# Performance work log

Measured on AMD Instinct MI355X. Metric: run time of the kernel, lower is better.

## Reference

```python
import jax, jax.numpy as jnp
import numpy as np
import math

B, T = 8, 16
CODE_NUM = 1024
CODE_SIZE = 48
GRAPH_SIZE = 32
HIDDEN = 150      # hidden_size == t_output_size
T_ATTN = 32       # t_attention_size
DP_ATTN = 32      # DotProductAttention size
OUT = 1024


def _lin(k, fan_in, fan_out):
    s = 1.0 / math.sqrt(fan_in)
    kw, kb = jax.random.split(k)
    W = jax.random.uniform(kw, (fan_in, fan_out), minval=-s, maxval=s, dtype=jnp.float32)
    b = jax.random.uniform(kb, (fan_out,), minval=-s, maxval=s, dtype=jnp.float32)
    return W, b


def setup_inputs():
    key = jax.random.key(0)
    ks = jax.random.split(key, 16)
    u = jax.random.uniform(ks[0], (B, T, CODE_NUM))
    m1 = (u < 0.03).astype(jnp.float32)                   # persistent codes
    m2 = ((u >= 0.03) & (u < 0.05)).astype(jnp.float32)   # emerging neighbor codes
    m3 = ((u >= 0.05) & (u < 0.06)).astype(jnp.float32)   # emerging unrelated codes
    divided = jnp.stack([m1, m2, m3], axis=-1)            # [B,T,N,3], disjoint
    code_x = jnp.clip(m1 + m2 + m3, 0.0, 1.0)             # current-visit codes
    neighbors = ((u >= 0.06) & (u < 0.12)).astype(jnp.float32)
    lens = jax.random.randint(ks[1], (B,), T // 2, T + 1)
    a = (jax.random.uniform(ks[2], (CODE_NUM, CODE_NUM)) < 0.01).astype(jnp.float32)
    adj = a / (a.sum(axis=1, keepdims=True) + 1e-6)
    c_emb = jax.random.normal(ks[3], (CODE_NUM, CODE_SIZE)) * 0.05
    n_emb = jax.random.normal(ks[4], (CODE_NUM, CODE_SIZE)) * 0.05
    u_emb = jax.random.normal(ks[5], (CODE_NUM, GRAPH_SIZE)) * 0.05
    Wg, bg = _lin(ks[6], CODE_SIZE, GRAPH_SIZE)           # GraphLayer dense
    Wi, bi = _lin(ks[7], GRAPH_SIZE, 3 * HIDDEN)          # GRUCell input (r|z|n)
    Wh, bh = _lin(ks[8], HIDDEN, 3 * HIDDEN)              # GRUCell hidden (r|z|n)
    Wq, bq = _lin(ks[9], GRAPH_SIZE, T_ATTN)
    Wk, bk = _lin(ks[10], GRAPH_SIZE, T_ATTN)
    Wv, bv = _lin(ks[11], GRAPH_SIZE, HIDDEN)
    Wd, bd = _lin(ks[12], HIDDEN, DP_ATTN)                # DotProductAttention dense
    context = jax.random.normal(ks[13], (DP_ATTN,)) * 0.1
    Wc, bc = _lin(ks[14], HIDDEN, OUT)                    # Classifier
    return dict(code_x=code_x, divided=divided, neighbors=neighbors, lens=lens,
                adj=adj, c_emb=c_emb, n_emb=n_emb, u_emb=u_emb, Wg=Wg, bg=bg,
                Wi=Wi, bi=bi, Wh=Wh, bh=bh, Wq=Wq, bq=bq, Wk=Wk, bk=bk,
                Wv=Wv, bv=bv, Wd=Wd, bd=bd, context=context, Wc=Wc, bc=bc)


def _forward(code_x, divided, neighbors, lens, adj, c_emb, n_emb, u_emb,
             Wg, bg, Wi, bi, Wh, bh, Wq, bq, Wk, bk, Wv, bv, Wd, bd, context, Wc, bc):
    Bb, Tt, N = code_x.shape
    H = Wh.shape[0]
    NEG = -1e30
    scale = 1.0 / math.sqrt(Wq.shape[1])

    def step(carry, xs):
        h_prev, no_prev = carry                 # [B,N,H], [B,N,G]
        c_t, d_t, n_t, t_idx = xs               # [B,N], [B,N,3], [B,N], scalar
        c = c_t[..., None]
        nb = n_t[..., None]
        # GraphLayer: masked embeddings + one-hop adjacency aggregation
        ce = c * c_emb                           # [B,N,C]
        ne = nb * n_emb
        adj_ce = jnp.einsum('mn,bnc->bmc', adj, ce)
        adj_ne = jnp.einsum('mn,bnc->bmc', adj, ne)
        co = jax.nn.leaky_relu((ce + c * adj_ce + c * adj_ne) @ Wg + bg)      # [B,N,G]
        no = jax.nn.leaky_relu((ne + nb * adj_ne + nb * adj_ce) @ Wg + bg)

        m1 = d_t[..., 0]; m2 = d_t[..., 1]; m3 = d_t[..., 2]
        # TransitionLayer part 1: GRUCell on persistent (m1) codes; h_new starts at 0
        gi = co @ Wi + bi
        gh = h_prev @ Wh + bh
        i_r, i_z, i_n = jnp.split(gi, 3, axis=-1)
        h_r, h_z, h_n = jnp.split(gh, 3, axis=-1)
        r = jax.nn.sigmoid(i_r + h_r)
        z = jax.nn.sigmoid(i_z + h_z)
        n_g = jnp.tanh(i_n + r * h_n)
        h_m1 = (1.0 - z) * n_g + z * h_prev
        h_new = jnp.where(m1[..., None] > 0, h_m1, 0.0)

        # TransitionLayer part 2: single-head attention over emerging (m2|m3) codes, t>0
        m23 = (m2 + m3) > 0
        qrows = jnp.where(m2[..., None] > 0, no_prev,
                          jnp.where(m3[..., None] > 0, u_emb, 0.0))           # [B,N,G]
        q = qrows @ Wq + bq
        k = co @ Wk + bk
        v = qrows @ Wv + bv
        s = jnp.einsum('bia,bja->bij', q, k) * scale
        s = jnp.where(m23[:, None, :], s, NEG)   # keys restricted to m2|m3 set
        h_m23 = jnp.tanh(jnp.einsum('bij,bjh->bih', jax.nn.softmax(s, axis=-1), v))
        use23 = t_idx > 0
        h_new = jnp.where(jnp.logical_and(use23, m23)[..., None], h_m23, h_new)

        # per-step output: max-pool over each active subset (0 if subset empty)
        om1 = jnp.max(jnp.where(m1[..., None] > 0, h_m1, NEG), axis=1)
        om1 = jnp.where(jnp.any(m1 > 0, axis=1)[:, None], om1, 0.0)
        om23 = jnp.max(jnp.where(m23[..., None], h_m23, NEG), axis=1)
        om23 = jnp.where(jnp.logical_and(use23, jnp.any(m23, axis=1))[:, None], om23, 0.0)
        return (h_new, no), om1 + om23

    h0 = jnp.zeros((Bb, N, H), code_x.dtype)
    no0 = jnp.zeros((Bb, N, Wg.shape[1]), code_x.dtype)
    xs = (jnp.moveaxis(code_x, 1, 0), jnp.moveaxis(divided, 1, 0),
          jnp.moveaxis(neighbors, 1, 0), jnp.arange(Tt))
    _, outs = jax.lax.scan(step, (h0, no0), xs)
    outs = jnp.moveaxis(outs, 0, 1)              # [B,T,H]

    # DotProductAttention over (ragged) visit axis
    vu = (outs @ Wd + bd) @ context              # [B,T]
    tmask = jnp.arange(Tt)[None, :] < lens[:, None]
    score = jax.nn.softmax(jnp.where(tmask, vu, NEG), axis=-1)
    pooled = jnp.einsum('bth,bt->bh', outs, score)
    # Classifier (dropout_rate=0 -> identity) with sigmoid activation
    return jax.nn.sigmoid(pooled @ Wc + bc)


def reference(code_x, divided, neighbors, lens, adj, c_emb, n_emb, u_emb,
              Wg, bg, Wi, bi, Wh, bh, Wq, bq, Wk, bk, Wv, bv, Wd, bd, context, Wc, bc):
    return _forward(code_x, divided, neighbors, lens, adj, c_emb, n_emb, u_emb,
                    Wg, bg, Wi, bi, Wh, bh, Wq, bq, Wk, bk, Wv, bv, Wd, bd,
                    context, Wc, bc)
```

## Files before the change

kernel.cpp:

```cpp
#include <hip/hip_runtime.h>
#include <hip/hip_bf16.h>

#define Bq   8
#define Tq   16
#define Nq   1024
#define Cq   48
#define Gq   32
#define Hq   150
#define H3q  450
#define TAq  32
#define OUTq 1024
#define BTq  128

#define NC_CAP 128
#define NM_CAP 64
#define NACT   (2 * NC_CAP)
#define MTILE  16
#define NMH    (NM_CAP / 2)

__device__ __forceinline__ float lrelu(float x){ return x > 0.f ? x : 0.01f * x; }
__device__ __forceinline__ float sigm(float x){ return 1.f / (1.f + expf(-x)); }

__device__ int   g_n1[BTq], g_n23[BTq], g_nchain[BTq], g_nchain2[BTq];
__device__ short g_list1[BTq][NM_CAP];
__device__ short g_list23[BTq][NM_CAP];
__device__ short g_mapc[BTq][Nq];
__device__ short g_mapn[BTq][Nq];
__device__ int   g_chain[BTq][NM_CAP];
__device__ int   g_chain2[BTq][NM_CAP];
__device__ unsigned char g_cls[BTq][NM_CAP];
__device__ float g_Pc[Nq][Gq];
__device__ float g_Pn[Nq][Gq];
__device__ float g_co[BTq][NC_CAP][Gq];
__device__ float g_no[BTq][NC_CAP][Gq];
__device__ float g_hm23[BTq][NM_CAP][Hq];
__device__ float g_om23p2[2][BTq][Hq];
__device__ float g_hm1[BTq][NM_CAP][Hq];
__device__ float g_om1p2[2][BTq][Hq];
__device__ float g_om1c[BTq][Hq];

__device__ __forceinline__ void gi3(const float* co_row, const float* Wi, const float* bi, int h,
                                    float& gr, float& gz, float& gn){
    gr = bi[h]; gz = bi[Hq + h]; gn = bi[2 * Hq + h];
    #pragma unroll
    for (int g = 0; g < Gq; ++g){
        float c = co_row[g];
        const float* w = Wi + g * H3q + h;
        gr += c * w[0];
        gz += c * w[Hq];
        gn += c * w[2 * Hq];
    }
}

__global__ __launch_bounds__(256) void k_pre(const float* c_emb, const float* n_emb, const float* Wg){
    int idx   = blockIdx.x * 256 + threadIdx.x;
    int which = idx >> 15;
    int r     = (idx >> 5) & 1023;
    int g     = idx & 31;
    const float* emb = which ? n_emb : c_emb;
    float acc = 0.f;
    for (int c = 0; c < Cq; ++c)
        acc += emb[r * Cq + c] * Wg[c * Gq + g];
    if (which) g_Pn[r][g] = acc; else g_Pc[r][g] = acc;
}

__global__ __launch_bounds__(512) void k_co(const float* code_x, const float* neighbors,
                                            const float* adj, const float* bg){
    int bt = blockIdx.x >> 1, half = blockIdx.x & 1, tid = threadIdx.x;
    __shared__ unsigned char cf_s[Nq], nf_s[Nq];
    __shared__ short lc_s[NC_CAP], ln_s[NC_CAP];
    __shared__ short act_s[NACT];
    __shared__ int nc_s, nn_s;
    __shared__ float Pact_s[NACT][Gq];
    __shared__ float A_s[MTILE][NACT];
    __shared__ short mrow_s[MTILE];
    int wave = tid >> 6, lane = tid & 63;

    for (int n = tid; n < Nq; n += 512){
        cf_s[n] = (code_x[bt * Nq + n]    > 0.f) ? 1 : 0;
        nf_s[n] = (neighbors[bt * Nq + n] > 0.f) ? 1 : 0;
    }
    __syncthreads();
    if (wave == 0){
        int base = 0;
        for (int start = 0; start < Nq; start += 64){
            int n = start + lane;
            int pred = cf_s[n];
            unsigned long long mm = __ballot(pred != 0);
            int pos = base + (int)__popcll(mm & ((1ull << lane) - 1ull));
            if (pred && pos < NC_CAP) lc_s[pos] = (short)n;
            base += (int)__popcll(mm);
        }
        if (lane == 0) nc_s = min(base, NC_CAP);
    } else if (wave == 1){
        int base = 0;
        for (int start = 0; start < Nq; start += 64){
            int n = start + lane;
            int pred = nf_s[n];
            unsigned long long mm = __ballot(pred != 0);
            int pos = base + (int)__popcll(mm & ((1ull << lane) - 1ull));
            if (pred && pos < NC_CAP) ln_s[pos] = (short)n;
            base += (int)__popcll(mm);
        }
        if (lane == 0) nn_s = min(base, NC_CAP);
    } else {
        if (half == 0) for (int n = tid - 128; n < Nq; n += 384) g_mapc[bt][n] = -1;
        else           for (int n = tid - 128; n < Nq; n += 384) g_mapn[bt][n] = -1;
    }
    __syncthreads();
    int nc = nc_s, nn = nn_s, total = nc + nn;

    for (int i = tid; i < total; i += 512) act_s[i] = (i < nc) ? lc_s[i] : ln_s[i - nc];
    if (half == 0) for (int i = tid; i < nc; i += 512) g_mapc[bt][lc_s[i]] = (short)i;
    else           for (int i = tid; i < nn; i += 512) g_mapn[bt][ln_s[i]] = (short)i;
    __syncthreads();

    for (int idx = tid; idx < total * Gq; idx += 512){
        int i = idx >> 5, g = idx & 31;
        Pact_s[i][g] = (i < nc) ? g_Pc[act_s[i]][g] : g_Pn[act_s[i]][g];
    }
    __syncthreads();

    int g = tid & 31, grp = tid >> 5;
    float bgv = bg[g];
    for (int rbase = half; rbase < total; rbase += 2 * MTILE){
        if (tid < MTILE){
            int r = rbase + 2 * tid;
            mrow_s[tid] = (r < total) ? act_s[r] : 0;
        }
        __syncthreads();
        int ntile = min(MTILE, (total - rbase + 1) / 2);
        for (int idx = tid; idx < ntile * total; idx += 512){
            int ti = idx / total, j = idx % total;
            A_s[ti][j] = adj[(size_t)mrow_s[ti] * Nq + act_s[j]];
        }
        __syncthreads();
        if (grp < ntile){
            int r = rbase + 2 * grp;
            float agg = 0.f;
            #pragma unroll 4
            for (int j = 0; j < total; ++j) agg += A_s[grp][j] * Pact_s[j][g];
            float v = lrelu(Pact_s[r][g] + agg + bgv);
            if (r < nc) g_co[bt][r][g]      = v;
            else        g_no[bt][r - nc][g] = v;
        }
        __syncthreads();
    }
}

__global__ __launch_bounds__(512) void k_mid(const float* divided, const float* u_emb,
                                             const float* Wk, const float* bk,
                                             const float* Wq_, const float* bq_,
                                             const float* Wv_, const float* bv_,
                                             const float* bg){
    int bt = blockIdx.x >> 1, half = blockIdx.x & 1, tid = threadIdx.x;
    int t = bt % Tq, btp = bt - 1;
    __shared__ unsigned char f1_s[Nq], f2_s[Nq], f3_s[Nq];
    __shared__ short l1_s[NM_CAP], l23_s[NM_CAP];
    __shared__ unsigned char wm_s[NMH];
    __shared__ int n1_s, n23_s;
    __shared__ float co23_s[NM_CAP][Gq];
    __shared__ float qr_s[NM_CAP][Gq];
    __shared__ float q_s[NMH][TAq + 1];
    __shared__ float k_s[NM_CAP][TAq + 1];
    __shared__ float s_s[NMH][NM_CAP + 1];
    __shared__ float vv_s[NM_CAP][Hq];
    __shared__ float hm_s[NMH][Hq];
    int wave = tid >> 6, lane = tid & 63;

    for (int idx = tid; idx < Nq * 3; idx += 512){
        float v = divided[(size_t)bt * Nq * 3 + idx];
        int n = idx / 3, c = idx - n * 3;
        unsigned char f = (v > 0.f) ? 1 : 0;
        if (c == 0) f1_s[n] = f;
        else if (c == 1) f2_s[n] = f;
        else f3_s[n] = f;
    }
    __syncthreads();
    if (wave == 0){
        int base = 0;
        for (int start = 0; start < Nq; start += 64){
            int n = start + lane;
            int pred = f1_s[n];
            unsigned long long mm = __ballot(pred != 0);
            int pos = base + (int)__popcll(mm & ((1ull << lane) - 1ull));
            if (pred && pos < NM_CAP) l1_s[pos] = (short)n;
            base += (int)__popcll(mm);
        }
        if (lane == 0) n1_s = min(base, NM_CAP);
    } else if (wave == 1){
        int base = 0;
        for (int start = 0; start < Nq; start += 64){
            int n = start + lane;
            int m2 = f2_s[n], m3 = f3_s[n];
            int pred = m2 | m3;
            unsigned long long mm = __ballot(pred != 0);
            int pos = base + (int)__popcll(mm & ((1ull << lane) - 1ull));
            if (pred && pos < NM_CAP) l23_s[pos] = (short)(n | (m2 ? 0x400 : 0));
            base += (int)__popcll(mm);
        }
        if (lane == 0) n23_s = min(base, NM_CAP);
    }
    __syncthreads();
    int n1 = n1_s, n23 = n23_s;
    if (half == 0){
        for (int i = tid; i < n1;  i += 512) g_list1[bt][i]  = l1_s[i];
        for (int i = tid; i < n23; i += 512) g_list23[bt][i] = l23_s[i];
        if (tid == 0){ g_n1[bt] = n1; g_n23[bt] = n23; }
    }
    if (t == 0 || n23 == 0) return;
    int nMy = (n23 > half) ? ((n23 - half + 1) >> 1) : 0;

    for (int il = tid; il < nMy; il += 512){
        int row = l23_s[2 * il + half] & 1023;
        unsigned char wm = 0;
        if (t < Tq - 1) wm = (divided[((size_t)(bt + 1) * Nq + row) * 3] > 0.f) ? 1 : 0;
        wm_s[il] = wm;
    }
    for (int idx = tid; idx < n23 * Gq; idx += 512){
        int i = idx >> 5, g = idx & 31;
        co23_s[i][g] = g_co[bt][g_mapc[bt][l23_s[i] & 1023]][g];
    }
    for (int idx = tid; idx < n23 * Gq; idx += 512){
        int i = idx >> 5, g = idx & 31;
        int e = l23_s[i], row = e & 1023;
        float qv;
        if (e & 0x400){
            int slot = g_mapn[btp][row];
            qv = (slot >= 0) ? g_no[btp][slot][g] : lrelu(bg[g]);
        } else {
            qv = u_emb[row * Gq + g];
        }
        qr_s[i][g] = qv;
    }
    __syncthreads();
    for (int idx = tid; idx < n23 * TAq; idx += 512){
        int i = idx >> 5, a = idx & 31;
        float acck = bk[a];
        #pragma unroll
        for (int g = 0; g < Gq; ++g) acck += co23_s[i][g] * Wk[g * TAq + a];
        k_s[i][a] = acck;
    }
    for (int idx = tid; idx < nMy * TAq; idx += 512){
        int il = idx >> 5, a = idx & 31;
        int i = 2 * il + half;
        float accq = bq_[a];
        #pragma unroll
        for (int g = 0; g < Gq; ++g) accq += qr_s[i][g] * Wq_[g * TAq + a];
        q_s[il][a] = accq;
    }
    for (int idx = tid; idx < n23 * Hq; idx += 512){
        int i = idx / Hq, h = idx % Hq;
        float acc = bv_[h];
        #pragma unroll
        for (int g = 0; g < Gq; ++g) acc += qr_s[i][g] * Wv_[g * Hq + h];
        vv_s[i][h] = acc;
    }
    __syncthreads();

    const float scale = 0.17677669529663687f;
    for (int idx = tid; idx < nMy * n23; idx += 512){
        int il = idx / n23, j = idx % n23;
        float acc = 0.f;
        #pragma unroll
        for (int a = 0; a < TAq; ++a) acc += q_s[il][a] * k_s[j][a];
        s_s[il][j] = acc * scale;
    }
    __syncthreads();
    for (int il = tid; il < nMy; il += 512){
        float mx = -1e30f;
        for (int j = 0; j < n23; ++j) mx = fmaxf(mx, s_s[il][j]);
        float sum = 0.f;
        for (int j = 0; j < n23; ++j){ float e = expf(s_s[il][j] - mx); s_s[il][j] = e; sum += e; }
        float inv = 1.f / sum;
        for (int j = 0; j < n23; ++j) s_s[il][j] *= inv;
    }
    __syncthreads();
    for (int idx = tid; idx < nMy * Hq; idx += 512){
        int il = idx / Hq, h = idx % Hq;
        float acc = 0.f;
        for (int j = 0; j < n23; ++j) acc += s_s[il][j] * vv_s[j][h];
        hm_s[il][h] = tanhf(acc);
    }
    __syncthreads();
    for (int idx = tid; idx < nMy * Hq; idx += 512){
        int il = idx / Hq, h = idx % Hq;
        if (wm_s[il]) g_hm23[bt][2 * il + half][h] = hm_s[il][h];
    }
    for (int h = tid; h < Hq; h += 512){
        float mx = -1e30f;
        for (int il = 0; il < nMy; ++il) mx = fmaxf(mx, hm_s[il][h]);
        g_om23p2[half][bt][h] = mx;
    }
}

__global__ __launch_bounds__(512) void k_gru1(const float* Wi, const float* bi,
                                              const float* Wh, const float* bh){
    int bt = blockIdx.x >> 1, half = blockIdx.x & 1, tid = threadIdx.x;
    int t = bt % Tq, btp = bt - 1;
    __shared__ short map1p[Nq], map23p[Nq];
    __shared__ short l1_s[NM_CAP];
    __shared__ unsigned char cls_s[NM_CAP];
    __shared__ int m23l_s[NM_CAP];
    __shared__ int nf23_s;
    __shared__ float co1_s[NMH][Gq];
    __shared__ float hb_s[Hq];
    __shared__ float ghf_s[H3q];
    __shared__ float gi_s[NMH][H3q];
    int n1 = g_n1[bt];
    int nMy = (n1 > half) ? ((n1 - half + 1) >> 1) : 0;
    for (int n = tid; n < Nq; n += 512){ map1p[n] = -1; map23p[n] = -1; }
    for (int i = tid; i < n1; i += 512) l1_s[i] = g_list1[bt][i];
    __syncthreads();
    if (t >= 1){
        int n1p = g_n1[btp];
        for (int i = tid; i < n1p; i += 512) map1p[g_list1[btp][i]] = (short)i;
        if (t >= 2){
            int n23p = g_n23[btp];
            for (int i = tid; i < n23p; i += 512) map23p[g_list23[btp][i] & 1023] = (short)i;
        }
    }
    __syncthreads();
    if (tid < 64){
        int i = tid;
        int cls = 0, sp = -1;
        if (i < n1 && t >= 1){
            int row = l1_s[i];
            if (map1p[row] >= 0){ cls = 1; sp = map1p[row]; }
            else if (t >= 2 && map23p[row] >= 0){ cls = 2; sp = map23p[row]; }
        }
        if (i < n1) cls_s[i] = (unsigned char)cls;
        if (half == 0 && i < n1) g_cls[bt][i] = (unsigned char)cls;
        unsigned long long mch = __ballot(cls == 1);
        unsigned long long m23 = __ballot(cls == 2 && (i & 1) == half);
        int pch = (int)__popcll(mch & ((1ull << i) - 1ull));
        int p23 = (int)__popcll(m23 & ((1ull << i) - 1ull));
        if (half == 0 && cls == 1) g_chain[bt][pch] = (i << 16) | sp;
        if (cls == 2 && (i & 1) == half) m23l_s[p23] = (i << 16) | sp;
        if (i == 0){
            nf23_s = (int)__popcll(m23);
            if (half == 0) g_nchain[bt] = (int)__popcll(mch);
        }
    }
    for (int idx = tid; idx < nMy * Gq; idx += 512){
        int il = idx >> 5, g = idx & 31;
        co1_s[il][g] = g_co[bt][g_mapc[bt][l1_s[2 * il + half]]][g];
    }
    __syncthreads();

    if (tid < H3q){
        float wcol[Gq];
        #pragma unroll
        for (int g = 0; g < Gq; ++g) wcol[g] = Wi[g * H3q + tid];
        float bij = bi[tid];
        for (int il = 0; il < nMy; ++il){
            float acc = bij;
            #pragma unroll
            for (int g = 0; g < Gq; ++g) acc += co1_s[il][g] * wcol[g];
            gi_s[il][tid] = acc;
        }
    }
    __syncthreads();

    for (int idx = tid; idx < nMy * Hq; idx += 512){
        int il = idx / Hq, h = idx % Hq;
        int i = 2 * il + half;
        if (cls_s[i] != 0) continue;
        float gr = gi_s[il][h], gz = gi_s[il][Hq + h], gn = gi_s[il][2 * Hq + h];
        float r  = sigm(gr + bh[h]);
        float z  = sigm(gz + bh[Hq + h]);
        float ng = tanhf(gn + r * bh[2 * Hq + h]);
        gi_s[il][h] = (1.f - z) * ng;
    }
    __syncthreads();

    int nf23 = nf23_s;
    for (int f = 0; f < nf23; ++f){
        int pk = m23l_s[f]; int i = pk >> 16, sp = pk & 0xffff;
        int il = i >> 1;
        for (int h = tid; h < Hq; h += 512) hb_s[h] = g_hm23[btp][sp][h];
        __syncthreads();
        for (int j = tid; j < H3q; j += 512){
            float acc = bh[j];
            for (int k2 = 0; k2 < Hq; ++k2) acc += hb_s[k2] * Wh[k2 * H3q + j];
            ghf_s[j] = acc;
        }
        __syncthreads();
        for (int h = tid; h < Hq; h += 512){
            float gr = gi_s[il][h], gz = gi_s[il][Hq + h], gn = gi_s[il][2 * Hq + h];
            float r  = sigm(gr + ghf_s[h]);
            float z  = sigm(gz + ghf_s[Hq + h]);
            float ng = tanhf(gn + r * ghf_s[2 * Hq + h]);
            gi_s[il][h] = (1.f - z) * ng + z * hb_s[h];
        }
        __syncthreads();
    }

    for (int idx = tid; idx < nMy * Hq; idx += 512){
        int il = idx / Hq, h = idx % Hq;
        int i = 2 * il + half;
        if (cls_s[i] != 1) g_hm1[bt][i][h] = gi_s[il][h];
    }
    for (int h = tid; h < Hq; h += 512){
        float mx = -1e30f;
        for (int il = 0; il < nMy; ++il)
            if (cls_s[2 * il + half] != 1) mx = fmaxf(mx, gi_s[il][h]);
        g_om1p2[half][bt][h] = mx;
    }
}

__global__ __launch_bounds__(512) void k_gru1b(const float* Wi, const float* bi,
                                               const float* Wh, const float* bh){
    int bt = blockIdx.x, tid = threadIdx.x;
    int t = bt % Tq, btp = bt - 1;
    __shared__ unsigned char defer_s[NM_CAP];
    __shared__ float co_s[Gq];
    __shared__ float hb_s[Hq];
    __shared__ float ghf_s[H3q];
    __shared__ float cmax_s[Hq];
    int nch = (t > 0) ? g_nchain[bt] : 0;
    for (int h = tid; h < Hq; h += 512) cmax_s[h] = -1e30f;
    if (tid < 64){
        int c = tid;
        int defer = 0;
        if (c < nch){
            int sp = g_chain[bt][c] & 0xffff;
            defer = (g_cls[btp][sp] == 1) ? 1 : 0;
            defer_s[c] = (unsigned char)defer;
        }
        unsigned long long md = __ballot((c < nch) && defer);
        int pos = (int)__popcll(md & ((1ull << c) - 1ull));
        if ((c < nch) && defer) g_chain2[bt][pos] = g_chain[bt][c];
        if (c == 0) g_nchain2[bt] = (int)__popcll(md);
    }
    __syncthreads();
    for (int c = 0; c < nch; ++c){
        if (defer_s[c]) continue;
        int pk = g_chain[bt][c]; int i = pk >> 16, sp = pk & 0xffff;
        if (tid < Gq) co_s[tid] = g_co[bt][g_mapc[bt][g_list1[bt][i]]][tid];
        for (int h = tid; h < Hq; h += 512) hb_s[h] = g_hm1[btp][sp][h];
        __syncthreads();
        for (int j = tid; j < H3q; j += 512){
            float acc = bh[j];
            for (int k2 = 0; k2 < Hq; ++k2) acc += hb_s[k2] * Wh[k2 * H3q + j];
            ghf_s[j] = acc;
        }
        __syncthreads();
        for (int h = tid; h < Hq; h += 512){
            float gr, gz, gn;
            gi3(co_s, Wi, bi, h, gr, gz, gn);
            float r  = sigm(gr + ghf_s[h]);
            float z  = sigm(gz + ghf_s[Hq + h]);
            float ng = tanhf(gn + r * ghf_s[2 * Hq + h]);
            float v  = (1.f - z) * ng + z * hb_s[h];
            g_hm1[bt][i][h] = v;
            cmax_s[h] = fmaxf(cmax_s[h], v);
        }
        __syncthreads();
    }
    for (int h = tid; h < Hq; h += 512) g_om1c[bt][h] = cmax_s[h];
}

__global__ __launch_bounds__(512) void k_gru2f(const float* Wi, const float* bi,
                                               const float* Wh, const float* bh,
                                               const int* lens, const float* Wd, const float* bd,
                                               const float* ctx, const float* Wc, const float* bc,
                                               float* out){
    int b = blockIdx.x, tid = threadIdx.x;
    __shared__ float co_s[Gq];
    __shared__ float hb_s[Hq];
    __shared__ float ghf_s[H3q];
    __shared__ float outs_s[Tq][Hq];
    __shared__ float wdc_s[Hq];
    __shared__ float score_s[Tq];
    __shared__ float pooled_s[Hq];
    for (int t = 1; t < Tq; ++t){
        int bt = b * Tq + t, btp = bt - 1;
        int nch2 = g_nchain2[bt];
        for (int c = 0; c < nch2; ++c){
            int pk = g_chain2[bt][c]; int i = pk >> 16, sp = pk & 0xffff;
            if (tid < Gq) co_s[tid] = g_co[bt][g_mapc[bt][g_list1[bt][i]]][tid];
            for (int h = tid; h < Hq; h += 512) hb_s[h] = g_hm1[btp][sp][h];
            __syncthreads();
            for (int j = tid; j < H3q; j += 512){
                float acc = bh[j];
                for (int k2 = 0; k2 < Hq; ++k2) acc += hb_s[k2] * Wh[k2 * H3q + j];
                ghf_s[j] = acc;
            }
            __syncthreads();
            for (int h = tid; h < Hq; h += 512){
                float gr, gz, gn;
                gi3(co_s, Wi, bi, h, gr, gz, gn);
                float r  = sigm(gr + ghf_s[h]);
                float z  = sigm(gz + ghf_s[Hq + h]);
                float ng = tanhf(gn + r * ghf_s[2 * Hq + h]);
                g_hm1[bt][i][h] = (1.f - z) * ng + z * hb_s[h];
            }
            __syncthreads();
        }
    }
    for (int idx = tid; idx < Tq * Hq; idx += 512){
        int t = idx / Hq, h = idx % Hq;
        int bt = b * Tq + t;
        int n1 = g_n1[bt], n23 = (t > 0) ? g_n23[bt] : 0;
        float o = 0.f;
        if (n1 > 0){
            float mx = fmaxf(fmaxf(g_om1p2[0][bt][h], g_om1p2[1][bt][h]), g_om1c[bt][h]);
            int nd = (t > 0) ? g_nchain2[bt] : 0;
            for (int c = 0; c < nd; ++c){
                int i = g_chain2[bt][c] >> 16;
                mx = fmaxf(mx, g_hm1[bt][i][h]);
            }
            o = mx;
        }
        if (n23 > 0) o += fmaxf(g_om23p2[0][bt][h], g_om23p2[1][bt][h]);
        outs_s[t][h] = o;
    }
    for (int h = tid; h < Hq; h += 512){
        float acc = 0.f;
        for (int d = 0; d < 32; ++d) acc += Wd[h * 32 + d] * ctx[d];
        wdc_s[h] = acc;
    }
    __syncthreads();
    int len = lens[b];
    if (tid < Tq){
        int t = tid;
        float acc = 0.f;
        for (int d = 0; d < 32; ++d) acc += bd[d] * ctx[d];
        for (int h = 0; h < Hq; ++h) acc += outs_s[t][h] * wdc_s[h];
        score_s[t] = (t < len) ? acc : -1e30f;
    }
    __syncthreads();
    if (tid == 0){
        float mx = -1e30f;
        for (int t = 0; t < Tq; ++t) mx = fmaxf(mx, score_s[t]);
        float sum = 0.f;
        for (int t = 0; t < Tq; ++t){ float e = expf(score_s[t] - mx); score_s[t] = e; sum += e; }
        float inv = 1.f / sum;
        for (int t = 0; t < Tq; ++t) score_s[t] *= inv;
    }
    __syncthreads();
    for (int h = tid; h < Hq; h += 512){
        float acc = 0.f;
        for (int t = 0; t < Tq; ++t) acc += score_s[t] * outs_s[t][h];
        pooled_s[h] = acc;
    }
    __syncthreads();
    for (int o = tid; o < OUTq; o += 512){
        float acc = bc[o];
        for (int h = 0; h < Hq; ++h) acc += pooled_s[h] * Wc[h * OUTq + o];
        out[b * OUTq + o] = sigm(acc);
    }
}

extern "C" void kernel_launch(void* const* d_in, const int* in_sizes, int n_in,
                              void* d_out, int out_size, void* d_ws, size_t ws_size,
                              hipStream_t stream){
    const float* code_x    = (const float*)d_in[0];
    const float* divided   = (const float*)d_in[1];
    const float* neighbors = (const float*)d_in[2];
    const int*   lens      = (const int*)  d_in[3];
    const float* adj       = (const float*)d_in[4];
    const float* c_emb     = (const float*)d_in[5];
    const float* n_emb     = (const float*)d_in[6];
    const float* u_emb     = (const float*)d_in[7];
    const float* Wg        = (const float*)d_in[8];
    const float* bg        = (const float*)d_in[9];
    const float* Wi        = (const float*)d_in[10];
    const float* bi        = (const float*)d_in[11];
    const float* Wh        = (const float*)d_in[12];
    const float* bh        = (const float*)d_in[13];
    const float* Wq_       = (const float*)d_in[14];
    const float* bq_       = (const float*)d_in[15];
    const float* Wk_       = (const float*)d_in[16];
    const float* bk_       = (const float*)d_in[17];
    const float* Wv_       = (const float*)d_in[18];
    const float* bv_       = (const float*)d_in[19];
    const float* Wd_       = (const float*)d_in[20];
    const float* bd_       = (const float*)d_in[21];
    const float* ctx       = (const float*)d_in[22];
    const float* Wc_       = (const float*)d_in[23];
    const float* bc_       = (const float*)d_in[24];
    float* out = (float*)d_out;

    hipLaunchKernelGGL(k_pre,   dim3(256),     dim3(256), 0, stream, c_emb, n_emb, Wg);
    hipLaunchKernelGGL(k_co,    dim3(2 * BTq), dim3(512), 0, stream, code_x, neighbors, adj, bg);
    hipLaunchKernelGGL(k_mid,   dim3(2 * BTq), dim3(512), 0, stream, divided, u_emb,
                       Wk_, bk_, Wq_, bq_, Wv_, bv_, bg);
    hipLaunchKernelGGL(k_gru1,  dim3(2 * BTq), dim3(512), 0, stream, Wi, bi, Wh, bh);
    hipLaunchKernelGGL(k_gru1b, dim3(BTq),     dim3(512), 0, stream, Wi, bi, Wh, bh);
    hipLaunchKernelGGL(k_gru2f, dim3(Bq),      dim3(512), 0, stream, Wi, bi, Wh, bh,
                       lens, Wd_, bd_, ctx, Wc_, bc_, out);
}
```

Before: 259.2 us.

## Fuse all stages into one persistent kernel with grid barriers

```diff
diff --git a/kernel.cpp b/kernel.cpp
--- a/kernel.cpp
+++ b/kernel.cpp
@@ -1,5 +1,4 @@
 #include <hip/hip_runtime.h>
-#include <hip/hip_bf16.h>
 
 #define Bq   8
 #define Tq   16
@@ -11,6 +10,7 @@
 #define TAq  32
 #define OUTq 1024
 #define BTq  128
+#define NBLK (2 * BTq)
 
 #define NC_CAP 128
 #define NM_CAP 64
@@ -29,8 +29,6 @@
 __device__ int   g_chain[BTq][NM_CAP];
 __device__ int   g_chain2[BTq][NM_CAP];
 __device__ unsigned char g_cls[BTq][NM_CAP];
-__device__ float g_Pc[Nq][Gq];
-__device__ float g_Pn[Nq][Gq];
 __device__ float g_co[BTq][NC_CAP][Gq];
 __device__ float g_no[BTq][NC_CAP][Gq];
 __device__ float g_hm23[BTq][NM_CAP][Hq];
@@ -38,6 +36,22 @@
 __device__ float g_hm1[BTq][NM_CAP][Hq];
 __device__ float g_om1p2[2][BTq][Hq];
 __device__ float g_om1c[BTq][Hq];
+
+__device__ unsigned long long g_bar_ctr = 0ull;
+
+__device__ __forceinline__ void grid_barrier(){
+    __syncthreads();
+    if (threadIdx.x == 0){
+        __threadfence();
+        unsigned long long old = atomicAdd(&g_bar_ctr, 1ull);
+        unsigned long long target = old - (old % (unsigned long long)NBLK) + (unsigned long long)NBLK;
+        while (__hip_atomic_load(&g_bar_ctr, __ATOMIC_RELAXED, __HIP_MEMORY_SCOPE_AGENT) < target){
+            __builtin_amdgcn_s_sleep(1);
+        }
+        __threadfence();
+    }
+    __syncthreads();
+}
 
 __device__ __forceinline__ void gi3(const float* co_row, const float* Wi, const float* bi, int h,
                                     float& gr, float& gz, float& gn){
@@ -52,504 +66,519 @@
     }
 }
 
-__global__ __launch_bounds__(256) void k_pre(const float* c_emb, const float* n_emb, const float* Wg){
-    int idx   = blockIdx.x * 256 + threadIdx.x;
-    int which = idx >> 15;
-    int r     = (idx >> 5) & 1023;
-    int g     = idx & 31;
-    const float* emb = which ? n_emb : c_emb;
-    float acc = 0.f;
-    for (int c = 0; c < Cq; ++c)
-        acc += emb[r * Cq + c] * Wg[c * Gq + g];
-    if (which) g_Pn[r][g] = acc; else g_Pc[r][g] = acc;
-}
-
-__global__ __launch_bounds__(512) void k_co(const float* code_x, const float* neighbors,
-                                            const float* adj, const float* bg){
-    int bt = blockIdx.x >> 1, half = blockIdx.x & 1, tid = threadIdx.x;
-    __shared__ unsigned char cf_s[Nq], nf_s[Nq];
-    __shared__ short lc_s[NC_CAP], ln_s[NC_CAP];
-    __shared__ short act_s[NACT];
-    __shared__ int nc_s, nn_s;
-    __shared__ float Pact_s[NACT][Gq];
-    __shared__ float A_s[MTILE][NACT];
-    __shared__ short mrow_s[MTILE];
-    int wave = tid >> 6, lane = tid & 63;
-
-    for (int n = tid; n < Nq; n += 512){
-        cf_s[n] = (code_x[bt * Nq + n]    > 0.f) ? 1 : 0;
-        nf_s[n] = (neighbors[bt * Nq + n] > 0.f) ? 1 : 0;
+union SharedU {
+    struct {
+        unsigned char cf[Nq], nf[Nq];
+        short lc[NC_CAP], ln[NC_CAP];
+        short act[NACT];
+        short mrow[MTILE];
+        float Wg[Cq][Gq];
+        float Pact[NACT][Gq];
+        float A[MTILE][NACT];
+    } co;
+    struct {
+        unsigned char f1[Nq], f2[Nq], f3[Nq];
+        short l1[NM_CAP], l23[NM_CAP];
+        unsigned char wm[NMH];
+        float co23[NM_CAP][Gq];
+        float qr[NM_CAP][Gq];
+        float q[NMH][TAq + 1];
+        float k[NM_CAP][TAq + 1];
+        float s[NMH][NM_CAP + 1];
+        float vv[NM_CAP][Hq];
+        float hm[NMH][Hq];
+    } mid;
+    struct {
+        short map1p[Nq], map23p[Nq];
+        short l1[NM_CAP];
+        unsigned char cls[NM_CAP];
+        int   m23l[NM_CAP];
+        float co1[NMH][Gq];
+        float hb[Hq];
+        float ghf[H3q];
+        float gi[NMH][H3q];
+    } g1;
+    struct {
+        unsigned char defer[NM_CAP];
+        float co[Gq];
+        float hb[Hq];
+        float ghf[H3q];
+        float cmax[Hq];
+    } g1b;
+    struct {
+        int   nch2[Tq];
+        float co[Gq];
+        float hb[Hq];
+        float ghf[H3q];
+        float outs[Tq][Hq];
+        float wdc[Hq];
+        float score[Tq];
+        float pooled[Hq];
+    } fin;
+};
+
+__global__ __launch_bounds__(512, 1) void k_fused(
+    const float* code_x, const float* divided, const float* neighbors,
+    const int* lens, const float* adj, const float* c_emb, const float* n_emb,
+    const float* u_emb, const float* Wg, const float* bg,
+    const float* Wi, const float* bi, const float* Wh, const float* bh,
+    const float* Wq_, const float* bq_, const float* Wk_, const float* bk_,
+    const float* Wv_, const float* bv_, const float* Wd, const float* bd,
+    const float* ctx, const float* Wc, const float* bc, float* out)
+{
+    __shared__ SharedU sh;
+    __shared__ int s_n0, s_n1v, s_i2;
+    const int tid = threadIdx.x;
+    const int blk = blockIdx.x;
+
+    {
+        int bt = blk >> 1, half = blk & 1;
+        int wave = tid >> 6, lane = tid & 63;
+        for (int n = tid; n < Nq; n += 512){
+            sh.co.cf[n] = (code_x[bt * Nq + n]    > 0.f) ? 1 : 0;
+            sh.co.nf[n] = (neighbors[bt * Nq + n] > 0.f) ? 1 : 0;
+        }
+        for (int i = tid; i < Cq * Gq; i += 512) (&sh.co.Wg[0][0])[i] = Wg[i];
+        __syncthreads();
+        if (wave == 0){
+            int base = 0;
+            for (int start = 0; start < Nq; start += 64){
+                int n = start + lane;
+                int pred = sh.co.cf[n];
+                unsigned long long mm = __ballot(pred != 0);
+                int pos = base + (int)__popcll(mm & ((1ull << lane) - 1ull));
+                if (pred && pos < NC_CAP) sh.co.lc[pos] = (short)n;
+                base += (int)__popcll(mm);
+            }
+            if (lane == 0) s_n0 = min(base, NC_CAP);
+        } else if (wave == 1){
+            int base = 0;
+            for (int start = 0; start < Nq; start += 64){
+                int n = start + lane;
+                int pred = sh.co.nf[n];
+                unsigned long long mm = __ballot(pred != 0);
+                int pos = base + (int)__popcll(mm & ((1ull << lane) - 1ull));
+                if (pred && pos < NC_CAP) sh.co.ln[pos] = (short)n;
+                base += (int)__popcll(mm);
+            }
+            if (lane == 0) s_n1v = min(base, NC_CAP);
+        } else {
+            if (half == 0) for (int n = tid - 128; n < Nq; n += 384) g_mapc[bt][n] = -1;
+            else           for (int n = tid - 128; n < Nq; n += 384) g_mapn[bt][n] = -1;
+        }
+        __syncthreads();
+        int nc = s_n0, nn = s_n1v, total = nc + nn;
+
+        for (int i = tid; i < total; i += 512) sh.co.act[i] = (i < nc) ? sh.co.lc[i] : sh.co.ln[i - nc];
+        if (half == 0) for (int i = tid; i < nc; i += 512) g_mapc[bt][sh.co.lc[i]] = (short)i;
+        else           for (int i = tid; i < nn; i += 512) g_mapn[bt][sh.co.ln[i]] = (short)i;
+        __syncthreads();
+
+        for (int idx = tid; idx < total * Gq; idx += 512){
+            int i = idx >> 5, g = idx & 31;
+            int row = sh.co.act[i];
+            const float* e = (i < nc) ? (c_emb + row * Cq) : (n_emb + row * Cq);
+            float acc = 0.f;
+            #pragma unroll
+            for (int c = 0; c < Cq; ++c) acc += e[c] * sh.co.Wg[c][g];
+            sh.co.Pact[i][g] = acc;
+        }
+        __syncthreads();
+
+        int g = tid & 31, grp = tid >> 5;
+        float bgv = bg[g];
+        for (int rbase = half; rbase < total; rbase += 2 * MTILE){
+            if (tid < MTILE){
+                int r = rbase + 2 * tid;
+                sh.co.mrow[tid] = (r < total) ? sh.co.act[r] : 0;
+            }
+            __syncthreads();
+            int ntile = min(MTILE, (total - rbase + 1) / 2);
+            for (int idx = tid; idx < ntile * total; idx += 512){
+                int ti = idx / total, j = idx % total;
+                sh.co.A[ti][j] = adj[(size_t)sh.co.mrow[ti] * Nq + sh.co.act[j]];
+            }
+            __syncthreads();
+            if (grp < ntile){
+                int r = rbase + 2 * grp;
+                float agg = 0.f;
+                #pragma unroll 4
+                for (int j = 0; j < total; ++j) agg += sh.co.A[grp][j] * sh.co.Pact[j][g];
+                float v = lrelu(sh.co.Pact[r][g] + agg + bgv);
+                if (r < nc) g_co[bt][r][g]      = v;
+                else        g_no[bt][r - nc][g] = v;
+            }
+            __syncthreads();
+        }
     }
-    __syncthreads();
-    if (wave == 0){
-        int base = 0;
-        for (int start = 0; start < Nq; start += 64){
-            int n = start + lane;
-            int pred = cf_s[n];
-            unsigned long long mm = __ballot(pred != 0);
-            int pos = base + (int)__popcll(mm & ((1ull << lane) - 1ull));
-            if (pred && pos < NC_CAP) lc_s[pos] = (short)n;
-            base += (int)__popcll(mm);
-        }
-        if (lane == 0) nc_s = min(base, NC_CAP);
-    } else if (wave == 1){
-        int base = 0;
-        for (int start = 0; start < Nq; start += 64){
-            int n = start + lane;
-            int pred = nf_s[n];
-            unsigned long long mm = __ballot(pred != 0);
-            int pos = base + (int)__popcll(mm & ((1ull << lane) - 1ull));
-            if (pred && pos < NC_CAP) ln_s[pos] = (short)n;
-            base += (int)__popcll(mm);
-        }
-        if (lane == 0) nn_s = min(base, NC_CAP);
-    } else {
-        if (half == 0) for (int n = tid - 128; n < Nq; n += 384) g_mapc[bt][n] = -1;
-        else           for (int n = tid - 128; n < Nq; n += 384) g_mapn[bt][n] = -1;
+    grid_barrier();
+
+    {
+        int bt = blk >> 1, half = blk & 1;
+        int t = bt % Tq, btp = bt - 1;
+        int wave = tid >> 6, lane = tid & 63;
+        for (int idx = tid; idx < Nq * 3; idx += 512){
+            float v = divided[(size_t)bt * Nq * 3 + idx];
+            int n = idx / 3, c = idx - n * 3;
+            unsigned char f = (v > 0.f) ? 1 : 0;
+            if (c == 0) sh.mid.f1[n] = f;
+            else if (c == 1) sh.mid.f2[n] = f;
+            else sh.mid.f3[n] = f;
+        }
+        __syncthreads();
+        if (wave == 0){
+            int base = 0;
+            for (int start = 0; start < Nq; start += 64){
+                int n = start + lane;
+                int pred = sh.mid.f1[n];
+                unsigned long long mm = __ballot(pred != 0);
+                int pos = base + (int)__popcll(mm & ((1ull << lane) - 1ull));
+                if (pred && pos < NM_CAP) sh.mid.l1[pos] = (short)n;
+                base += (int)__popcll(mm);
+            }
+            if (lane == 0) s_n0 = min(base, NM_CAP);
+        } else if (wave == 1){
+            int base = 0;
+            for (int start = 0; start < Nq; start += 64){
+                int n = start + lane;
+                int m2 = sh.mid.f2[n], m3 = sh.mid.f3[n];
+                int pred = m2 | m3;
+                unsigned long long mm = __ballot(pred != 0);
+                int pos = base + (int)__popcll(mm & ((1ull << lane) - 1ull));
+                if (pred && pos < NM_CAP) sh.mid.l23[pos] = (short)(n | (m2 ? 0x400 : 0));
+                base += (int)__popcll(mm);
+            }
+            if (lane == 0) s_n1v = min(base, NM_CAP);
+        }
+        __syncthreads();
+        int n1 = s_n0, n23 = s_n1v;
+        if (half == 0){
+            for (int i = tid; i < n1;  i += 512) g_list1[bt][i]  = sh.mid.l1[i];
+            for (int i = tid; i < n23; i += 512) g_list23[bt][i] = sh.mid.l23[i];
+            if (tid == 0){ g_n1[bt] = n1; g_n23[bt] = n23; }
+        }
+        if (t != 0 && n23 != 0){
+            int nMy = (n23 > half) ? ((n23 - half + 1) >> 1) : 0;
+
+            for (int il = tid; il < nMy; il += 512){
+                int row = sh.mid.l23[2 * il + half] & 1023;
+                unsigned char wmv = 0;
+                if (t < Tq - 1) wmv = (divided[((size_t)(bt + 1) * Nq + row) * 3] > 0.f) ? 1 : 0;
+                sh.mid.wm[il] = wmv;
+            }
+            for (int idx = tid; idx < n23 * Gq; idx += 512){
+                int i = idx >> 5, g = idx & 31;
+                sh.mid.co23[i][g] = g_co[bt][g_mapc[bt][sh.mid.l23[i] & 1023]][g];
+            }
+            for (int idx = tid; idx < n23 * Gq; idx += 512){
+                int i = idx >> 5, g = idx & 31;
+                int e = sh.mid.l23[i], row = e & 1023;
+                float qv;
+                if (e & 0x400){
+                    int slot = g_mapn[btp][row];
+                    qv = (slot >= 0) ? g_no[btp][slot][g] : lrelu(bg[g]);
+                } else {
+                    qv = u_emb[row * Gq + g];
+                }
+                sh.mid.qr[i][g] = qv;
+            }
+            __syncthreads();
+            for (int idx = tid; idx < n23 * TAq; idx += 512){
+                int i = idx >> 5, a = idx & 31;
+                float acck = bk_[a];
+                #pragma unroll
+                for (int g = 0; g < Gq; ++g) acck += sh.mid.co23[i][g] * Wk_[g * TAq + a];
+                sh.mid.k[i][a] = acck;
+            }
+            for (int idx = tid; idx < nMy * TAq; idx += 512){
+                int il = idx >> 5, a = idx & 31;
+                int i = 2 * il + half;
+                float accq = bq_[a];
+                #pragma unroll
+                for (int g = 0; g < Gq; ++g) accq += sh.mid.qr[i][g] * Wq_[g * TAq + a];
+                sh.mid.q[il][a] = accq;
+            }
+            for (int idx = tid; idx < n23 * Hq; idx += 512){
+                int i = idx / Hq, h = idx % Hq;
+                float acc = bv_[h];
+                #pragma unroll
+                for (int g = 0; g < Gq; ++g) acc += sh.mid.qr[i][g] * Wv_[g * Hq + h];
+                sh.mid.vv[i][h] = acc;
+            }
+            __syncthreads();
+
+            const float scale = 0.17677669529663687f;
+            for (int idx = tid; idx < nMy * n23; idx += 512){
+                int il = idx / n23, j = idx % n23;
+                float acc = 0.f;
+                #pragma unroll
+                for (int a = 0; a < TAq; ++a) acc += sh.mid.q[il][a] * sh.mid.k[j][a];
+                sh.mid.s[il][j] = acc * scale;
+            }
+            __syncthreads();
+            for (int il = tid; il < nMy; il += 512){
+                float mx = -1e30f;
+                for (int j = 0; j < n23; ++j) mx = fmaxf(mx, sh.mid.s[il][j]);
+                float sum = 0.f;
+                for (int j = 0; j < n23; ++j){ float e = expf(sh.mid.s[il][j] - mx); sh.mid.s[il][j] = e; sum += e; }
+                float inv = 1.f / sum;
+                for (int j = 0; j < n23; ++j) sh.mid.s[il][j] *= inv;
+            }
+            __syncthreads();
+            for (int idx = tid; idx < nMy * Hq; idx += 512){
+                int il = idx / Hq, h = idx % Hq;
+                float acc = 0.f;
+                for (int j = 0; j < n23; ++j) acc += sh.mid.s[il][j] * sh.mid.vv[j][h];
+                sh.mid.hm[il][h] = tanhf(acc);
+            }
+            __syncthreads();
+            for (int idx = tid; idx < nMy * Hq; idx += 512){
+                int il = idx / Hq, h = idx % Hq;
+                if (sh.mid.wm[il]) g_hm23[bt][2 * il + half][h] = sh.mid.hm[il][h];
+            }
+            for (int h = tid; h < Hq; h += 512){
+                float mx = -1e30f;
+                for (int il = 0; il < nMy; ++il) mx = fmaxf(mx, sh.mid.hm[il][h]);
+                g_om23p2[half][bt][h] = mx;
+            }
+        }
     }
-    __syncthreads();
-    int nc = nc_s, nn = nn_s, total = nc + nn;
-
-    for (int i = tid; i < total; i += 512) act_s[i] = (i < nc) ? lc_s[i] : ln_s[i - nc];
-    if (half == 0) for (int i = tid; i < nc; i += 512) g_mapc[bt][lc_s[i]] = (short)i;
-    else           for (int i = tid; i < nn; i += 512) g_mapn[bt][ln_s[i]] = (short)i;
-    __syncthreads();
-
-    for (int idx = tid; idx < total * Gq; idx += 512){
-        int i = idx >> 5, g = idx & 31;
-        Pact_s[i][g] = (i < nc) ? g_Pc[act_s[i]][g] : g_Pn[act_s[i]][g];
-    }
-    __syncthreads();
-
-    int g = tid & 31, grp = tid >> 5;
-    float bgv = bg[g];
-    for (int rbase = half; rbase < total; rbase += 2 * MTILE){
-        if (tid < MTILE){
-            int r = rbase + 2 * tid;
-            mrow_s[tid] = (r < total) ? act_s[r] : 0;
-        }
-        __syncthreads();
-        int ntile = min(MTILE, (total - rbase + 1) / 2);
-        for (int idx = tid; idx < ntile * total; idx += 512){
-            int ti = idx / total, j = idx % total;
-            A_s[ti][j] = adj[(size_t)mrow_s[ti] * Nq + act_s[j]];
-        }
-        __syncthreads();
-        if (grp < ntile){
-            int r = rbase + 2 * grp;
-            float agg = 0.f;
-            #pragma unroll 4
-            for (int j = 0; j < total; ++j) agg += A_s[grp][j] * Pact_s[j][g];
-            float v = lrelu(Pact_s[r][g] + agg + bgv);
-            if (r < nc) g_co[bt][r][g]      = v;
-            else        g_no[bt][r - nc][g] = v;
-        }
-        __syncthreads();
-    }
-}
-
-__global__ __launch_bounds__(512) void k_mid(const float* divided, const float* u_emb,
-                                             const float* Wk, const float* bk,
-                                             const float* Wq_, const float* bq_,
-                                             const float* Wv_, const float* bv_,
-                                             const float* bg){
-    int bt = blockIdx.x >> 1, half = blockIdx.x & 1, tid = threadIdx.x;
-    int t = bt % Tq, btp = bt - 1;
-    __shared__ unsigned char f1_s[Nq], f2_s[Nq], f3_s[Nq];
-    __shared__ short l1_s[NM_CAP], l23_s[NM_CAP];
-    __shared__ unsigned char wm_s[NMH];
-    __shared__ int n1_s, n23_s;
-    __shared__ float co23_s[NM_CAP][Gq];
-    __shared__ float qr_s[NM_CAP][Gq];
-    __shared__ float q_s[NMH][TAq + 1];
-    __shared__ float k_s[NM_CAP][TAq + 1];
-    __shared__ float s_s[NMH][NM_CAP + 1];
-    __shared__ float vv_s[NM_CAP][Hq];
-    __shared__ float hm_s[NMH][Hq];
-    int wave = tid >> 6, lane = tid & 63;
-
-    for (int idx = tid; idx < Nq * 3; idx += 512){
-        float v = divided[(size_t)bt * Nq * 3 + idx];
-        int n = idx / 3, c = idx - n * 3;
-        unsigned char f = (v > 0.f) ? 1 : 0;
-        if (c == 0) f1_s[n] = f;
-        else if (c == 1) f2_s[n] = f;
-        else f3_s[n] = f;
-    }
-    __syncthreads();
-    if (wave == 0){
-        int base = 0;
-        for (int start = 0; start < Nq; start += 64){
-            int n = start + lane;
-            int pred = f1_s[n];
-            unsigned long long mm = __ballot(pred != 0);
-            int pos = base + (int)__popcll(mm & ((1ull << lane) - 1ull));
-            if (pred && pos < NM_CAP) l1_s[pos] = (short)n;
-            base += (int)__popcll(mm);
-        }
-        if (lane == 0) n1_s = min(base, NM_CAP);
-    } else if (wave == 1){
-        int base = 0;
-        for (int start = 0; start < Nq; start += 64){
-            int n = start + lane;
-            int m2 = f2_s[n], m3 = f3_s[n];
-            int pred = m2 | m3;
-            unsigned long long mm = __ballot(pred != 0);
-            int pos = base + (int)__popcll(mm & ((1ull << lane) - 1ull));
-            if (pred && pos < NM_CAP) l23_s[pos] = (short)(n | (m2 ? 0x400 : 0));
-            base += (int)__popcll(mm);
-        }
-        if (lane == 0) n23_s = min(base, NM_CAP);
-    }
-    __syncthreads();
-    int n1 = n1_s, n23 = n23_s;
-    if (half == 0){
-        for (int i = tid; i < n1;  i += 512) g_list1[bt][i]  = l1_s[i];
-        for (int i = tid; i < n23; i += 512) g_list23[bt][i] = l23_s[i];
-        if (tid == 0){ g_n1[bt] = n1; g_n23[bt] = n23; }
-    }
-    if (t == 0 || n23 == 0) return;
-    int nMy = (n23 > half) ? ((n23 - half + 1) >> 1) : 0;
-
-    for (int il = tid; il < nMy; il += 512){
-        int row = l23_s[2 * il + half] & 1023;
-        unsigned char wm = 0;
-        if (t < Tq - 1) wm = (divided[((size_t)(bt + 1) * Nq + row) * 3] > 0.f) ? 1 : 0;
-        wm_s[il] = wm;
-    }
-    for (int idx = tid; idx < n23 * Gq; idx += 512){
-        int i = idx >> 5, g = idx & 31;
-        co23_s[i][g] = g_co[bt][g_mapc[bt][l23_s[i] & 1023]][g];
-    }
-    for (int idx = tid; idx < n23 * Gq; idx += 512){
-        int i = idx >> 5, g = idx & 31;
-        int e = l23_s[i], row = e & 1023;
-        float qv;
-        if (e & 0x400){
-            int slot = g_mapn[btp][row];
-            qv = (slot >= 0) ? g_no[btp][slot][g] : lrelu(bg[g]);
-        } else {
-            qv = u_emb[row * Gq + g];
-        }
-        qr_s[i][g] = qv;
-    }
-    __syncthreads();
-    for (int idx = tid; idx < n23 * TAq; idx += 512){
-        int i = idx >> 5, a = idx & 31;
-        float acck = bk[a];
-        #pragma unroll
-        for (int g = 0; g < Gq; ++g) acck += co23_s[i][g] * Wk[g * TAq + a];
-        k_s[i][a] = acck;
-    }
-    for (int idx = tid; idx < nMy * TAq; idx += 512){
-        int il = idx >> 5, a = idx & 31;
-        int i = 2 * il + half;
-        float accq = bq_[a];
-        #pragma unroll
-        for (int g = 0; g < Gq; ++g) accq += qr_s[i][g] * Wq_[g * TAq + a];
-        q_s[il][a] = accq;
-    }
-    for (int idx = tid; idx < n23 * Hq; idx += 512){
-        int i = idx / Hq, h = idx % Hq;
-        float acc = bv_[h];
-        #pragma unroll
-        for (int g = 0; g < Gq; ++g) acc += qr_s[i][g] * Wv_[g * Hq + h];
-        vv_s[i][h] = acc;
-    }
-    __syncthreads();
-
-    const float scale = 0.17677669529663687f;
-    for (int idx = tid; idx < nMy * n23; idx += 512){
-        int il = idx / n23, j = idx % n23;
-        float acc = 0.f;
-        #pragma unroll
-        for (int a = 0; a < TAq; ++a) acc += q_s[il][a] * k_s[j][a];
-        s_s[il][j] = acc * scale;
-    }
-    __syncthreads();
-    for (int il = tid; il < nMy; il += 512){
-        float mx = -1e30f;
-        for (int j = 0; j < n23; ++j) mx = fmaxf(mx, s_s[il][j]);
-        float sum = 0.f;
-        for (int j = 0; j < n23; ++j){ float e = expf(s_s[il][j] - mx); s_s[il][j] = e; sum += e; }
-        float inv = 1.f / sum;
-        for (int j = 0; j < n23; ++j) s_s[il][j] *= inv;
-    }
-    __syncthreads();
-    for (int idx = tid; idx < nMy * Hq; idx += 512){
-        int il = idx / Hq, h = idx % Hq;
-        float acc = 0.f;
-        for (int j = 0; j < n23; ++j) acc += s_s[il][j] * vv_s[j][h];
-        hm_s[il][h] = tanhf(acc);
-    }
-    __syncthreads();
-    for (int idx = tid; idx < nMy * Hq; idx += 512){
-        int il = idx / Hq, h = idx % Hq;
-        if (wm_s[il]) g_hm23[bt][2 * il + half][h] = hm_s[il][h];
-    }
-    for (int h = tid; h < Hq; h += 512){
-        float mx = -1e30f;
-        for (int il = 0; il < nMy; ++il) mx = fmaxf(mx, hm_s[il][h]);
-        g_om23p2[half][bt][h] = mx;
-    }
-}
-
-__global__ __launch_bounds__(512) void k_gru1(const float* Wi, const float* bi,
-                                              const float* Wh, const float* bh){
-    int bt = blockIdx.x >> 1, half = blockIdx.x & 1, tid = threadIdx.x;
-    int t = bt % Tq, btp = bt - 1;
-    __shared__ short map1p[Nq], map23p[Nq];
-    __shared__ short l1_s[NM_CAP];
-    __shared__ unsigned char cls_s[NM_CAP];
-    __shared__ int m23l_s[NM_CAP];
-    __shared__ int nf23_s;
-    __shared__ float co1_s[NMH][Gq];
-    __shared__ float hb_s[Hq];
-    __shared__ float ghf_s[H3q];
-    __shared__ float gi_s[NMH][H3q];
-    int n1 = g_n1[bt];
-    int nMy = (n1 > half) ? ((n1 - half + 1) >> 1) : 0;
-    for (int n = tid; n < Nq; n += 512){ map1p[n] = -1; map23p[n] = -1; }
-    for (int i = tid; i < n1; i += 512) l1_s[i] = g_list1[bt][i];
-    __syncthreads();
-    if (t >= 1){
-        int n1p = g_n1[btp];
-        for (int i = tid; i < n1p; i += 512) map1p[g_list1[btp][i]] = (short)i;
-        if (t >= 2){
-            int n23p = g_n23[btp];
-            for (int i = tid; i < n23p; i += 512) map23p[g_list23[btp][i] & 1023] = (short)i;
-        }
-    }
-    __syncthreads();
-    if (tid < 64){
-        int i = tid;
-        int cls = 0, sp = -1;
-        if (i < n1 && t >= 1){
-            int row = l1_s[i];
-            if (map1p[row] >= 0){ cls = 1; sp = map1p[row]; }
-            else if (t >= 2 && map23p[row] >= 0){ cls = 2; sp = map23p[row]; }
-        }
-        if (i < n1) cls_s[i] = (unsigned char)cls;
-        if (half == 0 && i < n1) g_cls[bt][i] = (unsigned char)cls;
-        unsigned long long mch = __ballot(cls == 1);
-        unsigned long long m23 = __ballot(cls == 2 && (i & 1) == half);
-        int pch = (int)__popcll(mch & ((1ull << i) - 1ull));
-        int p23 = (int)__popcll(m23 & ((1ull << i) - 1ull));
-        if (half == 0 && cls == 1) g_chain[bt][pch] = (i << 16) | sp;
-        if (cls == 2 && (i & 1) == half) m23l_s[p23] = (i << 16) | sp;
-        if (i == 0){
-            nf23_s = (int)__popcll(m23);
-            if (half == 0) g_nchain[bt] = (int)__popcll(mch);
-        }
-    }
-    for (int idx = tid; idx < nMy * Gq; idx += 512){
-        int il = idx >> 5, g = idx & 31;
-        co1_s[il][g] = g_co[bt][g_mapc[bt][l1_s[2 * il + half]]][g];
-    }
-    __syncthreads();
-
-    if (tid < H3q){
-        float wcol[Gq];
-        #pragma unroll
-        for (int g = 0; g < Gq; ++g) wcol[g] = Wi[g * H3q + tid];
-        float bij = bi[tid];
-        for (int il = 0; il < nMy; ++il){
-            float acc = bij;
+    grid_barrier();
+
+    {
+        int bt = blk >> 1, half = blk & 1;
+        int t = bt % Tq, btp = bt - 1;
+        int n1 = g_n1[bt];
+        int nMy = (n1 > half) ? ((n1 - half + 1) >> 1) : 0;
+        for (int n = tid; n < Nq; n += 512){ sh.g1.map1p[n] = -1; sh.g1.map23p[n] = -1; }
+        for (int i = tid; i < n1; i += 512) sh.g1.l1[i] = g_list1[bt][i];
+        __syncthreads();
+        if (t >= 1){
+            int n1p = g_n1[btp];
+            for (int i = tid; i < n1p; i += 512) sh.g1.map1p[g_list1[btp][i]] = (short)i;
+            if (t >= 2){
+                int n23p = g_n23[btp];
+                for (int i = tid; i < n23p; i += 512) sh.g1.map23p[g_list23[btp][i] & 1023] = (short)i;
+            }
+        }
+        __syncthreads();
+        if (tid < 64){
+            int i = tid;
+            int cls = 0, sp = -1;
+            if (i < n1 && t >= 1){
+                int row = sh.g1.l1[i];
+                if (sh.g1.map1p[row] >= 0){ cls = 1; sp = sh.g1.map1p[row]; }
+                else if (t >= 2 && sh.g1.map23p[row] >= 0){ cls = 2; sp = sh.g1.map23p[row]; }
+            }
+            if (i < n1) sh.g1.cls[i] = (unsigned char)cls;
+            if (half == 0 && i < n1) g_cls[bt][i] = (unsigned char)cls;
+            unsigned long long mch = __ballot(cls == 1);
+            unsigned long long m23 = __ballot(cls == 2 && (i & 1) == half);
+            int pch = (int)__popcll(mch & ((1ull << i) - 1ull));
+            int p23 = (int)__popcll(m23 & ((1ull << i) - 1ull));
+            if (half == 0 && cls == 1) g_chain[bt][pch] = (i << 16) | sp;
+            if (cls == 2 && (i & 1) == half) sh.g1.m23l[p23] = (i << 16) | sp;
+            if (i == 0){
+                s_i2 = (int)__popcll(m23);
+                if (half == 0) g_nchain[bt] = (int)__popcll(mch);
+            }
+        }
+        for (int idx = tid; idx < nMy * Gq; idx += 512){
+            int il = idx >> 5, g = idx & 31;
+            sh.g1.co1[il][g] = g_co[bt][g_mapc[bt][sh.g1.l1[2 * il + half]]][g];
+        }
+        __syncthreads();
+
+        if (tid < H3q){
+            float wcol[Gq];
             #pragma unroll
-            for (int g = 0; g < Gq; ++g) acc += co1_s[il][g] * wcol[g];
-            gi_s[il][tid] = acc;
-        }
-    }
-    __syncthreads();
-
-    for (int idx = tid; idx < nMy * Hq; idx += 512){
-        int il = idx / Hq, h = idx % Hq;
-        int i = 2 * il + half;
-        if (cls_s[i] != 0) continue;
-        float gr = gi_s[il][h], gz = gi_s[il][Hq + h], gn = gi_s[il][2 * Hq + h];
-        float r  = sigm(gr + bh[h]);
-        float z  = sigm(gz + bh[Hq + h]);
-        float ng = tanhf(gn + r * bh[2 * Hq + h]);
-        gi_s[il][h] = (1.f - z) * ng;
-    }
-    __syncthreads();
-
-    int nf23 = nf23_s;
-    for (int f = 0; f < nf23; ++f){
-        int pk = m23l_s[f]; int i = pk >> 16, sp = pk & 0xffff;
-        int il = i >> 1;
-        for (int h = tid; h < Hq; h += 512) hb_s[h] = g_hm23[btp][sp][h];
-        __syncthreads();
-        for (int j = tid; j < H3q; j += 512){
-            float acc = bh[j];
-            for (int k2 = 0; k2 < Hq; ++k2) acc += hb_s[k2] * Wh[k2 * H3q + j];
-            ghf_s[j] = acc;
-        }
-        __syncthreads();
-        for (int h = tid; h < Hq; h += 512){
-            float gr = gi_s[il][h], gz = gi_s[il][Hq + h], gn = gi_s[il][2 * Hq + h];
-            float r  = sigm(gr + ghf_s[h]);
-            float z  = sigm(gz + ghf_s[Hq + h]);
-            float ng = tanhf(gn + r * ghf_s[2 * Hq + h]);
-            gi_s[il][h] = (1.f - z) * ng + z * hb_s[h];
-        }
-        __syncthreads();
-    }
-
-    for (int idx = tid; idx < nMy * Hq; idx += 512){
-        int il = idx / Hq, h = idx % Hq;
-        int i = 2 * il + half;
-        if (cls_s[i] != 1) g_hm1[bt][i][h] = gi_s[il][h];
-    }
-    for (int h = tid; h < Hq; h += 512){
-        float mx = -1e30f;
-        for (int il = 0; il < nMy; ++il)
-            if (cls_s[2 * il + half] != 1) mx = fmaxf(mx, gi_s[il][h]);
-        g_om1p2[half][bt][h] = mx;
-    }
-}
-
-__global__ __launch_bounds__(512) void k_gru1b(const float* Wi, const float* bi,
-                                               const float* Wh, const float* bh){
-    int bt = blockIdx.x, tid = threadIdx.x;
-    int t = bt % Tq, btp = bt - 1;
-    __shared__ unsigned char defer_s[NM_CAP];
-    __shared__ float co_s[Gq];
-    __shared__ float hb_s[Hq];
-    __shared__ float ghf_s[H3q];
-    __shared__ float cmax_s[Hq];
-    int nch = (t > 0) ? g_nchain[bt] : 0;
-    for (int h = tid; h < Hq; h += 512) cmax_s[h] = -1e30f;
-    if (tid < 64){
-        int c = tid;
-        int defer = 0;
-        if (c < nch){
-            int sp = g_chain[bt][c] & 0xffff;
-            defer = (g_cls[btp][sp] == 1) ? 1 : 0;
-            defer_s[c] = (unsigned char)defer;
-        }
-        unsigned long long md = __ballot((c < nch) && defer);
-        int pos = (int)__popcll(md & ((1ull << c) - 1ull));
-        if ((c < nch) && defer) g_chain2[bt][pos] = g_chain[bt][c];
-        if (c == 0) g_nchain2[bt] = (int)__popcll(md);
-    }
-    __syncthreads();
-    for (int c = 0; c < nch; ++c){
-        if (defer_s[c]) continue;
-        int pk = g_chain[bt][c]; int i = pk >> 16, sp = pk & 0xffff;
-        if (tid < Gq) co_s[tid] = g_co[bt][g_mapc[bt][g_list1[bt][i]]][tid];
-        for (int h = tid; h < Hq; h += 512) hb_s[h] = g_hm1[btp][sp][h];
-        __syncthreads();
-        for (int j = tid; j < H3q; j += 512){
-            float acc = bh[j];
-            for (int k2 = 0; k2 < Hq; ++k2) acc += hb_s[k2] * Wh[k2 * H3q + j];
-            ghf_s[j] = acc;
-        }
-        __syncthreads();
-        for (int h = tid; h < Hq; h += 512){
-            float gr, gz, gn;
-            gi3(co_s, Wi, bi, h, gr, gz, gn);
-            float r  = sigm(gr + ghf_s[h]);
-            float z  = sigm(gz + ghf_s[Hq + h]);
-            float ng = tanhf(gn + r * ghf_s[2 * Hq + h]);
-            float v  = (1.f - z) * ng + z * hb_s[h];
-            g_hm1[bt][i][h] = v;
-            cmax_s[h] = fmaxf(cmax_s[h], v);
-        }
-        __syncthreads();
-    }
-    for (int h = tid; h < Hq; h += 512) g_om1c[bt][h] = cmax_s[h];
-}
-
-__global__ __launch_bounds__(512) void k_gru2f(const float* Wi, const float* bi,
-                                               const float* Wh, const float* bh,
-                                               const int* lens, const float* Wd, const float* bd,
-                                               const float* ctx, const float* Wc, const float* bc,
-                                               float* out){
-    int b = blockIdx.x, tid = threadIdx.x;
-    __shared__ float co_s[Gq];
-    __shared__ float hb_s[Hq];
-    __shared__ float ghf_s[H3q];
-    __shared__ float outs_s[Tq][Hq];
-    __shared__ float wdc_s[Hq];
-    __shared__ float score_s[Tq];
-    __shared__ float pooled_s[Hq];
-    for (int t = 1; t < Tq; ++t){
-        int bt = b * Tq + t, btp = bt - 1;
-        int nch2 = g_nchain2[bt];
-        for (int c = 0; c < nch2; ++c){
-            int pk = g_chain2[bt][c]; int i = pk >> 16, sp = pk & 0xffff;
-            if (tid < Gq) co_s[tid] = g_co[bt][g_mapc[bt][g_list1[bt][i]]][tid];
-            for (int h = tid; h < Hq; h += 512) hb_s[h] = g_hm1[btp][sp][h];
+            for (int g = 0; g < Gq; ++g) wcol[g] = Wi[g * H3q + tid];
+            float bij = bi[tid];
+            for (int il = 0; il < nMy; ++il){
+                float acc = bij;
+                #pragma unroll
+                for (int g = 0; g < Gq; ++g) acc += sh.g1.co1[il][g] * wcol[g];
+                sh.g1.gi[il][tid] = acc;
+            }
+        }
+        __syncthreads();
+
+        for (int idx = tid; idx < nMy * Hq; idx += 512){
+            int il = idx / Hq, h = idx % Hq;
+            int i = 2 * il + half;
+            if (sh.g1.cls[i] != 0) continue;
+            float gr = sh.g1.gi[il][h], gz = sh.g1.gi[il][Hq + h], gn = sh.g1.gi[il][2 * Hq + h];
+            float r  = sigm(gr + bh[h]);
+            float z  = sigm(gz + bh[Hq + h]);
+            float ng = tanhf(gn + r * bh[2 * Hq + h]);
+            sh.g1.gi[il][h] = (1.f - z) * ng;
+        }
+        __syncthreads();
+
+        int nf23 = s_i2;
+        for (int f = 0; f < nf23; ++f){
+            int pk = sh.g1.m23l[f]; int i = pk >> 16, sp = pk & 0xffff;
+            int il = i >> 1;
+            for (int h = tid; h < Hq; h += 512) sh.g1.hb[h] = g_hm23[btp][sp][h];
             __syncthreads();
             for (int j = tid; j < H3q; j += 512){
                 float acc = bh[j];
-                for (int k2 = 0; k2 < Hq; ++k2) acc += hb_s[k2] * Wh[k2 * H3q + j];
-                ghf_s[j] = acc;
+                for (int k2 = 0; k2 < Hq; ++k2) acc += sh.g1.hb[k2] * Wh[k2 * H3q + j];
+                sh.g1.ghf[j] = acc;
+            }
+            __syncthreads();
+            for (int h = tid; h < Hq; h += 512){
+                float gr = sh.g1.gi[il][h], gz = sh.g1.gi[il][Hq + h], gn = sh.g1.gi[il][2 * Hq + h];
+                float r  = sigm(gr + sh.g1.ghf[h]);
+                float z  = sigm(gz + sh.g1.ghf[Hq + h]);
+                float ng = tanhf(gn + r * sh.g1.ghf[2 * Hq + h]);
+                sh.g1.gi[il][h] = (1.f - z) * ng + z * sh.g1.hb[h];
+            }
+            __syncthreads();
+        }
+
+        for (int idx = tid; idx < nMy * Hq; idx += 512){
+            int il = idx / Hq, h = idx % Hq;
+            int i = 2 * il + half;
+            if (sh.g1.cls[i] != 1) g_hm1[bt][i][h] = sh.g1.gi[il][h];
+        }
+        for (int h = tid; h < Hq; h += 512){
+            float mx = -1e30f;
+            for (int il = 0; il < nMy; ++il)
+                if (sh.g1.cls[2 * il + half] != 1) mx = fmaxf(mx, sh.g1.gi[il][h]);
+            g_om1p2[half][bt][h] = mx;
+        }
+    }
+    grid_barrier();
+
+    if (blk < BTq){
+        int bt = blk;
+        int t = bt % Tq, btp = bt - 1;
+        int nch = (t > 0) ? g_nchain[bt] : 0;
+        for (int h = tid; h < Hq; h += 512) sh.g1b.cmax[h] = -1e30f;
+        if (tid < 64){
+            int c = tid;
+            int defer = 0;
+            if (c < nch){
+                int sp = g_chain[bt][c] & 0xffff;
+                defer = (g_cls[btp][sp] == 1) ? 1 : 0;
+                sh.g1b.defer[c] = (unsigned char)defer;
+            }
+            unsigned long long md = __ballot((c < nch) && defer);
+            int pos = (int)__popcll(md & ((1ull << c) - 1ull));
+            if ((c < nch) && defer) g_chain2[bt][pos] = g_chain[bt][c];
+            if (c == 0) g_nchain2[bt] = (int)__popcll(md);
+        }
+        __syncthreads();
+        for (int c = 0; c < nch; ++c){
+            if (sh.g1b.defer[c]) continue;
+            int pk = g_chain[bt][c]; int i = pk >> 16, sp = pk & 0xffff;
+            if (tid < Gq) sh.g1b.co[tid] = g_co[bt][g_mapc[bt][g_list1[bt][i]]][tid];
+            for (int h = tid; h < Hq; h += 512) sh.g1b.hb[h] = g_hm1[btp][sp][h];
+            __syncthreads();
+            for (int j = tid; j < H3q; j += 512){
+                float acc = bh[j];
+                for (int k2 = 0; k2 < Hq; ++k2) acc += sh.g1b.hb[k2] * Wh[k2 * H3q + j];
+                sh.g1b.ghf[j] = acc;
             }
             __syncthreads();
             for (int h = tid; h < Hq; h += 512){
                 float gr, gz, gn;
-                gi3(co_s, Wi, bi, h, gr, gz, gn);
-                float r  = sigm(gr + ghf_s[h]);
-                float z  = sigm(gz + ghf_s[Hq + h]);
-                float ng = tanhf(gn + r * ghf_s[2 * Hq + h]);
-                g_hm1[bt][i][h] = (1.f - z) * ng + z * hb_s[h];
-            }
-            __syncthreads();
-        }
+                gi3(sh.g1b.co, Wi, bi, h, gr, gz, gn);
+                float r  = sigm(gr + sh.g1b.ghf[h]);
+                float z  = sigm(gz + sh.g1b.ghf[Hq + h]);
+                float ng = tanhf(gn + r * sh.g1b.ghf[2 * Hq + h]);
+                float v  = (1.f - z) * ng + z * sh.g1b.hb[h];
+                g_hm1[bt][i][h] = v;
+                sh.g1b.cmax[h] = fmaxf(sh.g1b.cmax[h], v);
+            }
+            __syncthreads();
+        }
+        for (int h = tid; h < Hq; h += 512) g_om1c[bt][h] = sh.g1b.cmax[h];
     }
-    for (int idx = tid; idx < Tq * Hq; idx += 512){
-        int t = idx / Hq, h = idx % Hq;
-        int bt = b * Tq + t;
-        int n1 = g_n1[bt], n23 = (t > 0) ? g_n23[bt] : 0;
-        float o = 0.f;
-        if (n1 > 0){
-            float mx = fmaxf(fmaxf(g_om1p2[0][bt][h], g_om1p2[1][bt][h]), g_om1c[bt][h]);
-            int nd = (t > 0) ? g_nchain2[bt] : 0;
-            for (int c = 0; c < nd; ++c){
-                int i = g_chain2[bt][c] >> 16;
-                mx = fmaxf(mx, g_hm1[bt][i][h]);
-            }
-            o = mx;
-        }
-        if (n23 > 0) o += fmaxf(g_om23p2[0][bt][h], g_om23p2[1][bt][h]);
-        outs_s[t][h] = o;
-    }
-    for (int h = tid; h < Hq; h += 512){
-        float acc = 0.f;
-        for (int d = 0; d < 32; ++d) acc += Wd[h * 32 + d] * ctx[d];
-        wdc_s[h] = acc;
-    }
-    __syncthreads();
-    int len = lens[b];
-    if (tid < Tq){
-        int t = tid;
-        float acc = 0.f;
-        for (int d = 0; d < 32; ++d) acc += bd[d] * ctx[d];
-        for (int h = 0; h < Hq; ++h) acc += outs_s[t][h] * wdc_s[h];
-        score_s[t] = (t < len) ? acc : -1e30f;
-    }
-    __syncthreads();
-    if (tid == 0){
-        float mx = -1e30f;
-        for (int t = 0; t < Tq; ++t) mx = fmaxf(mx, score_s[t]);
-        float sum = 0.f;
-        for (int t = 0; t < Tq; ++t){ float e = expf(score_s[t] - mx); score_s[t] = e; sum += e; }
-        float inv = 1.f / sum;
-        for (int t = 0; t < Tq; ++t) score_s[t] *= inv;
-    }
-    __syncthreads();
-    for (int h = tid; h < Hq; h += 512){
-        float acc = 0.f;
-        for (int t = 0; t < Tq; ++t) acc += score_s[t] * outs_s[t][h];
-        pooled_s[h] = acc;
-    }
-    __syncthreads();
-    for (int o = tid; o < OUTq; o += 512){
-        float acc = bc[o];
-        for (int h = 0; h < Hq; ++h) acc += pooled_s[h] * Wc[h * OUTq + o];
-        out[b * OUTq + o] = sigm(acc);
+    grid_barrier();
+
+    if (blk < Bq){
+        int b = blk;
+        if (tid < Tq) sh.fin.nch2[tid] = (tid > 0) ? g_nchain2[b * Tq + tid] : 0;
+        __syncthreads();
+        for (int t = 1; t < Tq; ++t){
+            int bt = b * Tq + t, btp = bt - 1;
+            int nch2 = sh.fin.nch2[t];
+            for (int c = 0; c < nch2; ++c){
+                int pk = g_chain2[bt][c]; int i = pk >> 16, sp = pk & 0xffff;
+                if (tid < Gq) sh.fin.co[tid] = g_co[bt][g_mapc[bt][g_list1[bt][i]]][tid];
+                for (int h = tid; h < Hq; h += 512) sh.fin.hb[h] = g_hm1[btp][sp][h];
+                __syncthreads();
+                for (int j = tid; j < H3q; j += 512){
+                    float acc = bh[j];
+                    for (int k2 = 0; k2 < Hq; ++k2) acc += sh.fin.hb[k2] * Wh[k2 * H3q + j];
+                    sh.fin.ghf[j] = acc;
+                }
+                __syncthreads();
+                for (int h = tid; h < Hq; h += 512){
+                    float gr, gz, gn;
+                    gi3(sh.fin.co, Wi, bi, h, gr, gz, gn);
+                    float r  = sigm(gr + sh.fin.ghf[h]);
+                    float z  = sigm(gz + sh.fin.ghf[Hq + h]);
+                    float ng = tanhf(gn + r * sh.fin.ghf[2 * Hq + h]);
+                    g_hm1[bt][i][h] = (1.f - z) * ng + z * sh.fin.hb[h];
+                }
+                __syncthreads();
+            }
+        }
+        for (int idx = tid; idx < Tq * Hq; idx += 512){
+            int t = idx / Hq, h = idx % Hq;
+            int bt = b * Tq + t;
+            int n1 = g_n1[bt], n23 = (t > 0) ? g_n23[bt] : 0;
+            float o = 0.f;
+            if (n1 > 0){
+                float mx = fmaxf(fmaxf(g_om1p2[0][bt][h], g_om1p2[1][bt][h]), g_om1c[bt][h]);
+                int nd = sh.fin.nch2[t];
+                for (int c = 0; c < nd; ++c){
+                    int i = g_chain2[bt][c] >> 16;
+                    mx = fmaxf(mx, g_hm1[bt][i][h]);
+                }
+                o = mx;
+            }
+            if (n23 > 0) o += fmaxf(g_om23p2[0][bt][h], g_om23p2[1][bt][h]);
+            sh.fin.outs[t][h] = o;
+        }
+        for (int h = tid; h < Hq; h += 512){
+            float acc = 0.f;
+            for (int d = 0; d < 32; ++d) acc += Wd[h * 32 + d] * ctx[d];
+            sh.fin.wdc[h] = acc;
+        }
+        __syncthreads();
+        int len = lens[b];
+        if (tid < Tq){
+            int t = tid;
+            float acc = 0.f;
+            for (int d = 0; d < 32; ++d) acc += bd[d] * ctx[d];
+            for (int h = 0; h < Hq; ++h) acc += sh.fin.outs[t][h] * sh.fin.wdc[h];
+            sh.fin.score[t] = (t < len) ? acc : -1e30f;
+        }
+        __syncthreads();
+        if (tid == 0){
+            float mx = -1e30f;
+            for (int t = 0; t < Tq; ++t) mx = fmaxf(mx, sh.fin.score[t]);
+            float sum = 0.f;
+            for (int t = 0; t < Tq; ++t){ float e = expf(sh.fin.score[t] - mx); sh.fin.score[t] = e; sum += e; }
+            float inv = 1.f / sum;
+            for (int t = 0; t < Tq; ++t) sh.fin.score[t] *= inv;
+        }
+        __syncthreads();
+        for (int h = tid; h < Hq; h += 512){
+            float acc = 0.f;
+            for (int t = 0; t < Tq; ++t) acc += sh.fin.score[t] * sh.fin.outs[t][h];
+            sh.fin.pooled[h] = acc;
+        }
+        __syncthreads();
+        for (int o = tid; o < OUTq; o += 512){
+            float acc = bc[o];
+            for (int h = 0; h < Hq; ++h) acc += sh.fin.pooled[h] * Wc[h * OUTq + o];
+            out[b * OUTq + o] = sigm(acc);
+        }
     }
 }
 
@@ -583,12 +612,8 @@
     const float* bc_       = (const float*)d_in[24];
     float* out = (float*)d_out;
 
-    hipLaunchKernelGGL(k_pre,   dim3(256),     dim3(256), 0, stream, c_emb, n_emb, Wg);
-    hipLaunchKernelGGL(k_co,    dim3(2 * BTq), dim3(512), 0, stream, code_x, neighbors, adj, bg);
-    hipLaunchKernelGGL(k_mid,   dim3(2 * BTq), dim3(512), 0, stream, divided, u_emb,
-                       Wk_, bk_, Wq_, bq_, Wv_, bv_, bg);
-    hipLaunchKernelGGL(k_gru1,  dim3(2 * BTq), dim3(512), 0, stream, Wi, bi, Wh, bh);
-    hipLaunchKernelGGL(k_gru1b, dim3(BTq),     dim3(512), 0, stream, Wi, bi, Wh, bh);
-    hipLaunchKernelGGL(k_gru2f, dim3(Bq),      dim3(512), 0, stream, Wi, bi, Wh, bh,
-                       lens, Wd_, bd_, ctx, Wc_, bc_, out);
+    hipLaunchKernelGGL(k_fused, dim3(NBLK), dim3(512), 0, stream,
+                       code_x, divided, neighbors, lens, adj, c_emb, n_emb, u_emb,
+                       Wg, bg, Wi, bi, Wh, bh, Wq_, bq_, Wk_, bk_, Wv_, bv_,
+                       Wd_, bd_, ctx, Wc_, bc_, out);
 }
```

Result: slower. 340.2 us (+31.2%).
